# Kernel tuning notes

Measured on AMD Instinct MI355X. Metric: run time of the kernel, lower is better.

Reference implementation:

```python
import jax, jax.numpy as jnp
import numpy as np

N, D, R, B, K = 16384, 300, 10, 1024, 64


def setup_inputs() -> dict:
    key = jax.random.key(0)
    ks = jax.random.split(key, 6)
    return {
        "node_feat_src": jax.random.normal(ks[0], (N, D), jnp.float32),
        "node_feat_tgt": jax.random.normal(ks[1], (N, D), jnp.float32),
        "srcs_index": jax.random.randint(ks[2], (B, K), 0, N),
        "tgts_index": jax.random.randint(ks[3], (B, K), 0, N),
        "src_vs": jax.random.normal(ks[4], (R, D), jnp.float32),
        "tgt_vs": jax.random.normal(ks[5], (R, D), jnp.float32),
    }


def _tower(h, vs):
    # Householder chain: h @ (I - v v^T / (v^T v)) == h - ((h v) / (v^T v)) v^T
    def step(h, v):
        coef = (h @ v) / (v @ v)  # [N]
        return h - coef[:, None] * v[None, :], None
    h, _ = jax.lax.scan(step, h, vs)
    return h


def _l2norm(x):
    # matches F.normalize(p=2, eps=1e-12) over the last dim
    n = jnp.linalg.norm(x, axis=-1, keepdims=True)
    return x / jnp.maximum(n, 1e-12)


def reference(node_feat_src, node_feat_tgt, srcs_index, tgts_index, src_vs, tgt_vs):
    src_h = _tower(node_feat_src, src_vs)  # [N, D]
    tgt_h = _tower(node_feat_tgt, tgt_vs)  # [N, D]

    pos_src = _l2norm(src_h[srcs_index[:, 0]])  # [B, D]
    pos_tgt = _l2norm(tgt_h[tgts_index[:, 0]])  # [B, D]
    src_list = _l2norm(src_h[srcs_index])       # [B, K, D]
    tgt_list = _l2norm(tgt_h[tgts_index])       # [B, K, D]

    sim_src2tgt = jnp.einsum('bd,bkd->bk', pos_src, tgt_list)  # [B, K]
    sim_tgt2src = jnp.einsum('bd,bkd->bk', pos_tgt, src_list)  # [B, K]

    # CSLS hubness penalties: mean of top-10 cross-domain cosine sims
    sim_matrix = _l2norm(src_h) @ _l2norm(tgt_h).T  # [N, N]
    rt = jnp.mean(jax.lax.top_k(sim_matrix, 10)[0], axis=1)    # [N]
    rs = jnp.mean(jax.lax.top_k(sim_matrix.T, 10)[0], axis=1)  # [N]

    srcs_rt = rt[srcs_index]  # [B, K]
    tgts_rs = rs[tgts_index]  # [B, K]

    logits_src2tgt = sim_src2tgt * 2 - srcs_rt[:, 0:1] - tgts_rs
    logits_tgt2src = sim_tgt2src * 2 - tgts_rs[:, 0:1] - srcs_rt
    return logits_src2tgt, logits_tgt2src
```

## Files before the change

### kernel.cpp

```cpp
#include <hip/hip_runtime.h>
#include <hip/hip_bf16.h>

#define NN 16384
#define DD 300
#define DP 320
#define RR 10
#define BB 1024
#define KK 64
#define CAP 128
#define CAPL 512

typedef __attribute__((ext_vector_type(8))) short s8v;
typedef __attribute__((ext_vector_type(4))) float f4v;
typedef _Float16 h2 __attribute__((ext_vector_type(2)));

__device__ __forceinline__ unsigned mono2(unsigned d) {
    unsigned s = ((d >> 15) & 0x10001u) * 0xFFFFu;
    return d ^ (s | 0x80008000u);
}
__device__ __forceinline__ float key2f16(unsigned k) {
    unsigned short b = (k & 0x8000u) ? (unsigned short)(k ^ 0x8000u)
                                     : (unsigned short)(~k & 0xFFFFu);
    _Float16 hv = __builtin_bit_cast(_Float16, b);
    return (float)hv;
}

__device__ __forceinline__ h2 h2max(h2 a, h2 b) {
    return __builtin_elementwise_max(a, b);
}
__device__ __forceinline__ h2 hmax2s(h2 a, int xb) {
    int x = __shfl_xor(__builtin_bit_cast(int, a), xb);
    return h2max(a, __builtin_bit_cast(h2, x));
}
__device__ __forceinline__ h2 packh2(float a, float b) {
    h2 r; r[0] = (_Float16)a; r[1] = (_Float16)b; return r;
}

__device__ __forceinline__ void ins10(unsigned (&lst)[10], unsigned v) {
    #pragma unroll
    for (int q = 0; q < 10; ++q) {
        unsigned a  = lst[q];
        unsigned mx = a > v ? a : v;
        v           = a > v ? v : a;
        lst[q] = mx;
    }
}
__device__ __forceinline__ void ins10f(float (&lst)[10], float v) {
    #pragma unroll
    for (int q = 0; q < 10; ++q) {
        float a  = lst[q];
        float mx = fmaxf(a, v);
        v        = fminf(a, v);
        lst[q] = mx;
    }
}

__device__ __forceinline__ void xcd_map(int bid, int& by, int& bx) {
    const int xcd = bid & 7;
    const int s   = bid >> 3;
    bx = (xcd << 2) | (s & 3);
    by = s >> 2;
}

__device__ __forceinline__ void gload_lds16(const void* g, void* l) {
#if __has_builtin(__builtin_amdgcn_global_load_lds)
    __builtin_amdgcn_global_load_lds(
        (const __attribute__((address_space(1))) void*)g,
        (__attribute__((address_space(3))) void*)l, 16, 0, 0);
#else
    const int lane = threadIdx.x & 63;
    int4 v = *reinterpret_cast<const int4*>(g);
    *reinterpret_cast<int4*>((char*)l + lane * 16) = v;
#endif
}

__device__ __forceinline__ void stage_tile(
        const __hip_bfloat16* __restrict__ Ab, const __hip_bfloat16* __restrict__ Bb,
        int kb, char* base, int w, int lane) {
    const int r8 = lane >> 3;
    const int u  = (lane & 7) ^ r8;
    const int row = w * 8 + r8;
    const size_t go = (size_t)row * DP + kb * 64 + u * 8;
    gload_lds16(Ab + go, base + w * 1024);
    gload_lds16(Bb + go, base + 16384 + w * 1024);
}

__global__ __launch_bounds__(256) void tower_kernel(
        const float* __restrict__ feat, const float* __restrict__ vs,
        __hip_bfloat16* __restrict__ out) {
    __shared__ float vsh[RR * DD];
    const int tid = threadIdx.x;
    for (int i = tid; i < RR * DD; i += 256) vsh[i] = vs[i];
    __syncthreads();

    const int lane = tid & 63;
    const int wave = tid >> 6;
    const int row  = blockIdx.x * 4 + wave;

    float h[5];
    #pragma unroll
    for (int j = 0; j < 5; ++j) {
        int d = lane + 64 * j;
        h[j] = (d < DD) ? feat[(size_t)row * DD + d] : 0.f;
    }
    #pragma unroll
    for (int r = 0; r < RR; ++r) {
        float vl[5];
        float hv = 0.f, vv = 0.f;
        #pragma unroll
        for (int j = 0; j < 5; ++j) {
            int d = lane + 64 * j;
            float v = (d < DD) ? vsh[r * DD + d] : 0.f;
            vl[j] = v;
            hv += h[j] * v;
            vv += v * v;
        }
        #pragma unroll
        for (int o = 32; o; o >>= 1) {
            hv += __shfl_xor(hv, o);
            vv += __shfl_xor(vv, o);
        }
        float coef = hv / vv;
        #pragma unroll
        for (int j = 0; j < 5; ++j) h[j] -= coef * vl[j];
    }
    float nn = 0.f;
    #pragma unroll
    for (int j = 0; j < 5; ++j) nn += h[j] * h[j];
    #pragma unroll
    for (int o = 32; o; o >>= 1) nn += __shfl_xor(nn, o);
    float scale = 1.f / fmaxf(sqrtf(nn), 1e-12f);
    #pragma unroll
    for (int j = 0; j < 5; ++j) {
        int d = lane + 64 * j;
        float val = (d < DD) ? h[j] * scale : 0.f;
        out[(size_t)row * DP + d] = __float2bfloat16(val);
    }
}

#define KLOOP(COMPUTE_BODY)                                                    \
    stage_tile(Ab, Bb, 0, u_lds, w, lane);                                     \
    _Pragma("unroll")                                                          \
    for (int kb = 0; kb < 5; ++kb) {                                           \
        char* curb = u_lds + (kb & 1) * 32768;                                 \
        if (kb < 4)                                                            \
            stage_tile(Ab, Bb, kb + 1, u_lds + ((kb + 1) & 1) * 32768, w, lane); \
        if (kb < 4) { asm volatile("s_waitcnt vmcnt(2)" ::: "memory"); }       \
        else        { asm volatile("s_waitcnt vmcnt(0)" ::: "memory"); }       \
        __builtin_amdgcn_s_barrier();                                          \
        asm volatile("" ::: "memory");                                         \
        {                                                                      \
            const __hip_bfloat16* Asub = (const __hip_bfloat16*)curb;          \
            const __hip_bfloat16* Bsub = (const __hip_bfloat16*)(curb + 16384);\
            COMPUTE_BODY                                                       \
        }                                                                      \
        asm volatile("" ::: "memory");                                         \
        __builtin_amdgcn_s_barrier();                                          \
    }

#define COMPUTE_TILE                                                           \
    _Pragma("unroll")                                                          \
    for (int ks = 0; ks < 2; ++ks) {                                           \
        s8v af[2], bfv[2];                                                     \
        const int ulog = ks * 4 + (lane >> 4);                                 \
        const int up   = ulog ^ (lane & 7);                                    \
        _Pragma("unroll")                                                      \
        for (int m = 0; m < 2; ++m) {                                          \
            const int row = wr * 32 + m * 16 + (lane & 15);                    \
            af[m] = *reinterpret_cast<const s8v*>(Asub + row * 64 + up * 8);   \
        }                                                                      \
        _Pragma("unroll")                                                      \
        for (int n = 0; n < 2; ++n) {                                          \
            const int row = wc * 32 + n * 16 + (lane & 15);                    \
            bfv[n] = *reinterpret_cast<const s8v*>(Bsub + row * 64 + up * 8);  \
        }                                                                      \
        _Pragma("unroll")                                                      \
        for (int m = 0; m < 2; ++m)                                            \
            _Pragma("unroll")                                                  \
            for (int n = 0; n < 2; ++n)                                        \
                acc[m][n] = __builtin_amdgcn_mfma_f32_16x16x32_bf16(           \
                    af[m], bfv[n], acc[m][n], 0, 0, 0);                        \
    }

__global__ __launch_bounds__(1024) void passA_kernel(
        const __hip_bfloat16* __restrict__ A, const __hip_bfloat16* __restrict__ Bm,
        unsigned short* __restrict__ rowsmax_g,
        unsigned short* __restrict__ colsmax_g) {
    __shared__ __align__(16) char u_lds[65536];
    __shared__ unsigned short rowsm[16][512];
    __shared__ unsigned short colsm[512][16];

    const int tid = threadIdx.x;
    const int lane = tid & 63;
    const int w = tid >> 6;
    const int wr = w >> 2, wc = w & 3;
    int by, bx; xcd_map(blockIdx.x, by, bx);
    const int i0 = by * 512, j0 = bx * 512;

    for (int ti = 0; ti < 4; ++ti) {
        for (int tj = 0; tj < 4; ++tj) {
            f4v acc[2][2];
            #pragma unroll
            for (int m = 0; m < 2; ++m)
                #pragma unroll
                for (int n = 0; n < 2; ++n)
                    acc[m][n] = (f4v){0.f, 0.f, 0.f, 0.f};

            const __hip_bfloat16* Ab = A  + (size_t)(i0 + ti * 128) * DP;
            const __hip_bfloat16* Bb = Bm + (size_t)(j0 + tj * 128) * DP;

            KLOOP(COMPUTE_TILE)

            #pragma unroll
            for (int m = 0; m < 2; ++m) {
                h2 a01 = h2max(packh2(acc[m][0][0], acc[m][0][1]),
                               packh2(acc[m][1][0], acc[m][1][1]));
                h2 a23 = h2max(packh2(acc[m][0][2], acc[m][0][3]),
                               packh2(acc[m][1][2], acc[m][1][3]));
                a01 = hmax2s(a01, 1); a23 = hmax2s(a23, 1);
                a01 = hmax2s(a01, 2); a23 = hmax2s(a23, 2);
                a01 = hmax2s(a01, 4); a23 = hmax2s(a23, 4);
                a01 = hmax2s(a01, 8); a23 = hmax2s(a23, 8);
                if ((lane & 15) == m * 8) {
                    const int rl = ti * 128 + wr * 32 + m * 16 + ((lane >> 4) << 2);
                    uint2 u = make_uint2(mono2(__builtin_bit_cast(unsigned, a01)),
                                         mono2(__builtin_bit_cast(unsigned, a23)));
                    *reinterpret_cast<uint2*>(&rowsm[tj * 4 + wc][rl]) = u;
                }
            }
            {
                float rm0 = -1e30f, rm1 = -1e30f;
                #pragma unroll
                for (int m = 0; m < 2; ++m) {
                    rm0 = fmaxf(rm0, fmaxf(fmaxf(acc[m][0][0], acc[m][0][1]),
                                           fmaxf(acc[m][0][2], acc[m][0][3])));
                    rm1 = fmaxf(rm1, fmaxf(fmaxf(acc[m][1][0], acc[m][1][1]),
                                           fmaxf(acc[m][1][2], acc[m][1][3])));
                }
                h2 c = packh2(rm0, rm1);
                c = hmax2s(c, 16);
                c = hmax2s(c, 32);
                if ((lane >> 4) == 0) {
                    const int s = ti * 4 + wr;
                    const int cb = tj * 128 + wc * 32 + (lane & 15);
                    unsigned k = mono2(__builtin_bit_cast(unsigned, c));
                    colsm[cb][s]      = (unsigned short)(k & 0xFFFFu);
                    colsm[cb + 16][s] = (unsigned short)(k >> 16);
                }
            }
        }
    }
    __syncthreads();
    if (tid < 512) {
        const int r = tid;
        unsigned short t16[16];
        #pragma unroll
        for (int s = 0; s < 16; ++s) t16[s] = rowsm[s][r];
        uint4 o0, o1;
        o0.x = t16[0] | ((unsigned)t16[1] << 16);  o0.y = t16[2] | ((unsigned)t16[3] << 16);
        o0.z = t16[4] | ((unsigned)t16[5] << 16);  o0.w = t16[6] | ((unsigned)t16[7] << 16);
        o1.x = t16[8] | ((unsigned)t16[9] << 16);  o1.y = t16[10] | ((unsigned)t16[11] << 16);
        o1.z = t16[12] | ((unsigned)t16[13] << 16); o1.w = t16[14] | ((unsigned)t16[15] << 16);
        uint4* rdst = reinterpret_cast<uint4*>(rowsmax_g + (size_t)(i0 + r) * 512 + bx * 16);
        rdst[0] = o0; rdst[1] = o1;
    } else {
        const int r = tid - 512;
        uint4 q0 = *reinterpret_cast<uint4*>(&colsm[r][0]);
        uint4 q1 = *reinterpret_cast<uint4*>(&colsm[r][8]);
        uint4* cdst = reinterpret_cast<uint4*>(colsmax_g + (size_t)(j0 + r) * 512 + by * 16);
        cdst[0] = q0; cdst[1] = q1;
    }
}

__global__ __launch_bounds__(256) void thresh_kernel(
        const unsigned short* __restrict__ rowsmax_g,
        const unsigned short* __restrict__ colsmax_g,
        float* __restrict__ Tlb_row, float* __restrict__ Tlb_col,
        unsigned* __restrict__ rowcnt, unsigned* __restrict__ colcnt) {
    const int t = blockIdx.x * 256 + threadIdx.x;
    const bool isRow = t < NN;
    const int idx = isRow ? t : t - NN;
    const unsigned short* src = (isRow ? rowsmax_g : colsmax_g) + (size_t)idx * 512;

    unsigned lst[10];
    #pragma unroll
    for (int q = 0; q < 10; ++q) lst[q] = 0u;

    const uint4* p = reinterpret_cast<const uint4*>(src);
    for (int c = 0; c < 64; ++c) {
        uint4 q = p[c];
        unsigned v0 = q.x & 0xFFFFu, v1 = q.x >> 16;
        unsigned v2 = q.y & 0xFFFFu, v3 = q.y >> 16;
        unsigned v4 = q.z & 0xFFFFu, v5 = q.z >> 16;
        unsigned v6 = q.w & 0xFFFFu, v7 = q.w >> 16;
        unsigned g01 = v0 > v1 ? v0 : v1, g23 = v2 > v3 ? v2 : v3;
        unsigned g45 = v4 > v5 ? v4 : v5, g67 = v6 > v7 ? v6 : v7;
        unsigned ga = g01 > g23 ? g01 : g23, gb = g45 > g67 ? g45 : g67;
        unsigned g = ga > gb ? ga : gb;
        if (g > lst[9]) {
            if (v0 > lst[9]) ins10(lst, v0);
            if (v1 > lst[9]) ins10(lst, v1);
            if (v2 > lst[9]) ins10(lst, v2);
            if (v3 > lst[9]) ins10(lst, v3);
            if (v4 > lst[9]) ins10(lst, v4);
            if (v5 > lst[9]) ins10(lst, v5);
            if (v6 > lst[9]) ins10(lst, v6);
            if (v7 > lst[9]) ins10(lst, v7);
        }
    }
    float f = key2f16(lst[9]);
    float lb = f - fabsf(f) * 0.002f - 1e-6f;
    if (isRow) { Tlb_row[idx] = lb; rowcnt[idx] = 0u; }
    else       { Tlb_col[idx] = lb; colcnt[idx] = 0u; }
}

__global__ __launch_bounds__(1024) void passB_kernel(
        const __hip_bfloat16* __restrict__ A, const __hip_bfloat16* __restrict__ Bm,
        const float* __restrict__ Tlb_row, const float* __restrict__ Tlb_col,
        unsigned* __restrict__ rowcnt, unsigned* __restrict__ colcnt,
        float* __restrict__ rowbuf, float* __restrict__ colbuf) {
    __shared__ __align__(16) char u_lds[65536];
    __shared__ float Trow_s[512];
    __shared__ float Tcol_s[512];
    __shared__ unsigned scnt[2];
    __shared__ uint2 sbuf[2][CAPL];

    const int tid = threadIdx.x;
    const int lane = tid & 63;
    const int w = tid >> 6;
    const int wr = w >> 2, wc = w & 3;
    int by, bx; xcd_map(blockIdx.x, by, bx);
    const int i0 = by * 512, j0 = bx * 512;

    if (tid < 512) Trow_s[tid] = Tlb_row[i0 + tid];
    else           Tcol_s[tid - 512] = Tlb_col[j0 + tid - 512];
    if (tid < 2) scnt[tid] = 0u;
    __syncthreads();

    for (int ti = 0; ti < 4; ++ti) {
        float trmin = 1e30f;
        #pragma unroll
        for (int m = 0; m < 2; ++m)
            #pragma unroll
            for (int r = 0; r < 4; ++r)
                trmin = fminf(trmin, Trow_s[ti * 128 + wr * 32 + m * 16 + ((lane >> 4) << 2) + r]);

        for (int tj = 0; tj < 4; ++tj) {
            f4v acc[2][2];
            #pragma unroll
            for (int m = 0; m < 2; ++m)
                #pragma unroll
                for (int n = 0; n < 2; ++n)
                    acc[m][n] = (f4v){0.f, 0.f, 0.f, 0.f};

            const __hip_bfloat16* Ab = A  + (size_t)(i0 + ti * 128) * DP;
            const __hip_bfloat16* Bb = Bm + (size_t)(j0 + tj * 128) * DP;

            KLOOP(COMPUTE_TILE)

            const int c0i = tj * 128 + wc * 32 + (lane & 15);
            const int c1i = c0i + 16;
            const float tc0 = Tcol_s[c0i], tc1 = Tcol_s[c1i];
            float vm = -1e30f;
            #pragma unroll
            for (int m = 0; m < 2; ++m) {
                float a = fmaxf(fmaxf(acc[m][0][0], acc[m][0][1]),
                                fmaxf(acc[m][0][2], acc[m][0][3]));
                float b = fmaxf(fmaxf(acc[m][1][0], acc[m][1][1]),
                                fmaxf(acc[m][1][2], acc[m][1][3]));
                vm = fmaxf(vm, fmaxf(a, b));
            }
            if (vm >= fminf(trmin, fminf(tc0, tc1))) {
                #pragma unroll
                for (int m = 0; m < 2; ++m) {
                    #pragma unroll
                    for (int r = 0; r < 4; ++r) {
                        const int rl = ti * 128 + wr * 32 + m * 16 + ((lane >> 4) << 2) + r;
                        const float T = Trow_s[rl];
                        const float v0 = acc[m][0][r], v1 = acc[m][1][r];
                        if (v0 >= T) {
                            unsigned p = atomicAdd(&scnt[0], 1u);
                            if (p < CAPL) sbuf[0][p] = make_uint2((unsigned)(i0 + rl), __float_as_uint(v0));
                            else { unsigned q = atomicAdd(&rowcnt[i0 + rl], 1u);
                                   if (q < CAP) rowbuf[(size_t)(i0 + rl) * CAP + q] = v0; }
                        }
                        if (v1 >= T) {
                            unsigned p = atomicAdd(&scnt[0], 1u);
                            if (p < CAPL) sbuf[0][p] = make_uint2((unsigned)(i0 + rl), __float_as_uint(v1));
                            else { unsigned q = atomicAdd(&rowcnt[i0 + rl], 1u);
                                   if (q < CAP) rowbuf[(size_t)(i0 + rl) * CAP + q] = v1; }
                        }
                        if (v0 >= tc0) {
                            unsigned p = atomicAdd(&scnt[1], 1u);
                            if (p < CAPL) sbuf[1][p] = make_uint2((unsigned)(j0 + c0i), __float_as_uint(v0));
                            else { unsigned q = atomicAdd(&colcnt[j0 + c0i], 1u);
                                   if (q < CAP) colbuf[(size_t)(j0 + c0i) * CAP + q] = v0; }
                        }
                        if (v1 >= tc1) {
                            unsigned p = atomicAdd(&scnt[1], 1u);
                            if (p < CAPL) sbuf[1][p] = make_uint2((unsigned)(j0 + c1i), __float_as_uint(v1));
                            else { unsigned q = atomicAdd(&colcnt[j0 + c1i], 1u);
                                   if (q < CAP) colbuf[(size_t)(j0 + c1i) * CAP + q] = v1; }
                        }
                    }
                }
            }
        }
    }

    __syncthreads();
    {
        const unsigned nr = scnt[0] < CAPL ? scnt[0] : CAPL;
        const unsigned nc = scnt[1] < CAPL ? scnt[1] : CAPL;
        for (unsigned i = tid; i < nr; i += 1024) {
            uint2 e = sbuf[0][i];
            unsigned p = atomicAdd(&rowcnt[e.x], 1u);
            if (p < CAP) rowbuf[(size_t)e.x * CAP + p] = __uint_as_float(e.y);
        }
        for (unsigned i = tid; i < nc; i += 1024) {
            uint2 e = sbuf[1][i];
            unsigned p = atomicAdd(&colcnt[e.x], 1u);
            if (p < CAP) colbuf[(size_t)e.x * CAP + p] = __uint_as_float(e.y);
        }
    }
}

__global__ __launch_bounds__(256) void final_kernel(
        const unsigned* __restrict__ rowcnt, const unsigned* __restrict__ colcnt,
        const float* __restrict__ rowbuf, const float* __restrict__ colbuf,
        float* __restrict__ rt, float* __restrict__ rs) {
    const int t = blockIdx.x * 256 + threadIdx.x;
    const bool isRow = t < NN;
    const int idx = isRow ? t : t - NN;
    const unsigned cn = (isRow ? rowcnt : colcnt)[idx];
    const int n = (int)(cn < CAP ? cn : CAP);
    const float* buf = (isRow ? rowbuf : colbuf) + (size_t)idx * CAP;

    float lst[10];
    #pragma unroll
    for (int q = 0; q < 10; ++q) lst[q] = -1e30f;
    for (int i = 0; i < n; ++i) {
        float v = buf[i];
        if (v > lst[9]) ins10f(lst, v);
    }
    float s = 0.f;
    #pragma unroll
    for (int q = 0; q < 10; ++q) s += lst[q];
    s *= 0.1f;
    (isRow ? rt : rs)[idx] = s;
}

__global__ __launch_bounds__(256) void logits_kernel(
        const __hip_bfloat16* __restrict__ srcH, const __hip_bfloat16* __restrict__ tgtH,
        const int* __restrict__ sidx, const int* __restrict__ tidx,
        const float* __restrict__ rt, const float* __restrict__ rs,
        float* __restrict__ out) {
    const int b    = blockIdx.x;
    const int lane = threadIdx.x & 63;
    const int w    = threadIdx.x >> 6;

    const int s0 = sidx[b * KK];
    const int t0 = tidx[b * KK];
    float ps[5], pt[5];
    #pragma unroll
    for (int j = 0; j < 5; ++j) {
        int d = lane + 64 * j;
        ps[j] = __bfloat162float(srcH[(size_t)s0 * DP + d]);
        pt[j] = __bfloat162float(tgtH[(size_t)t0 * DP + d]);
    }
    const float rt_s0 = rt[s0];
    const float rs_t0 = rs[t0];

    for (int kk = w; kk < KK; kk += 4) {
        const int it = tidx[b * KK + kk];
        const int is = sidx[b * KK + kk];
        float a = 0.f, c = 0.f;
        #pragma unroll
        for (int j = 0; j < 5; ++j) {
            int d = lane + 64 * j;
            a += ps[j] * __bfloat162float(tgtH[(size_t)it * DP + d]);
            c += pt[j] * __bfloat162float(srcH[(size_t)is * DP + d]);
        }
        #pragma unroll
        for (int o = 32; o; o >>= 1) {
            a += __shfl_xor(a, o);
            c += __shfl_xor(c, o);
        }
        if (lane == 0) {
            out[b * KK + kk]           = 2.f * a - rt_s0 - rs[it];
            out[BB * KK + b * KK + kk] = 2.f * c - rs_t0 - rt[is];
        }
    }
}

extern "C" void kernel_launch(void* const* d_in, const int* in_sizes, int n_in,
                              void* d_out, int out_size, void* d_ws, size_t ws_size,
                              hipStream_t stream) {
    const float* nf_src = (const float*)d_in[0];
    const float* nf_tgt = (const float*)d_in[1];
    const int*   sidx   = (const int*)d_in[2];
    const int*   tidx   = (const int*)d_in[3];
    const float* svs    = (const float*)d_in[4];
    const float* tvs    = (const float*)d_in[5];

    char* ws = (char*)d_ws;
    const size_t SZ_H  = (size_t)NN * DP * 2;
    const size_t SZ_SM = (size_t)NN * 512 * 2;
    __hip_bfloat16* srcH = (__hip_bfloat16*)ws;
    __hip_bfloat16* tgtH = (__hip_bfloat16*)(ws + SZ_H);
    unsigned short* rowsmax = (unsigned short*)(ws + 2 * SZ_H);
    unsigned short* colsmax = (unsigned short*)(ws + 2 * SZ_H + SZ_SM);
    float* rowbuf = (float*)(ws + 2 * SZ_H);
    float* colbuf = (float*)(ws + 2 * SZ_H + (size_t)NN * CAP * 4);
    char* tail = ws + 2 * SZ_H + 2 * SZ_SM;
    float* Tlb_row = (float*)(tail);
    float* Tlb_col = (float*)(tail + 65536);
    unsigned* rowcnt = (unsigned*)(tail + 2 * 65536);
    unsigned* colcnt = (unsigned*)(tail + 3 * 65536);
    float* rt = (float*)(tail + 4 * 65536);
    float* rs = (float*)(tail + 5 * 65536);

    tower_kernel<<<NN / 4, 256, 0, stream>>>(nf_src, svs, srcH);
    tower_kernel<<<NN / 4, 256, 0, stream>>>(nf_tgt, tvs, tgtH);
    passA_kernel<<<1024, 1024, 0, stream>>>(srcH, tgtH, rowsmax, colsmax);
    thresh_kernel<<<(2 * NN) / 256, 256, 0, stream>>>(rowsmax, colsmax, Tlb_row, Tlb_col,
                                                      rowcnt, colcnt);
    passB_kernel<<<1024, 1024, 0, stream>>>(srcH, tgtH, Tlb_row, Tlb_col,
                                            rowcnt, colcnt, rowbuf, colbuf);
    final_kernel<<<(2 * NN) / 256, 256, 0, stream>>>(rowcnt, colcnt, rowbuf, colbuf, rt, rs);
    logits_kernel<<<BB, 256, 0, stream>>>(srcH, tgtH, sidx, tidx, rt, rs, (float*)d_out);
}
```

Before: 632.8 us.

## Compute two column tiles per K-loop to reuse A tile and halve barriers

Both GEMM passes now process a pair of 128-column B tiles per K-loop iteration, staging A once alongside two B tiles in a larger double-buffered LDS region. This reuses A fragments across twice the MFMAs and halves the number of barrier-synchronised K-loops and A reloads. The cost is more accumulator registers and LDS per block (96KB staging plus existing buffers), which may pressure occupancy or exceed LDS limits alongside the other shared arrays.

```diff
diff --git a/kernel.cpp b/kernel.cpp
--- a/kernel.cpp
+++ b/kernel.cpp
@@ -9,6 +9,7 @@
 #define KK 64
 #define CAP 128
 #define CAPL 512
+#define BUFSZ 49152
 
 typedef __attribute__((ext_vector_type(8))) short s8v;
 typedef __attribute__((ext_vector_type(4))) float f4v;
@@ -74,15 +75,18 @@
 #endif
 }
 
-__device__ __forceinline__ void stage_tile(
-        const __hip_bfloat16* __restrict__ Ab, const __hip_bfloat16* __restrict__ Bb,
+__device__ __forceinline__ void stage_tile2(
+        const __hip_bfloat16* __restrict__ Ab,
+        const __hip_bfloat16* __restrict__ Bb0,
+        const __hip_bfloat16* __restrict__ Bb1,
         int kb, char* base, int w, int lane) {
     const int r8 = lane >> 3;
     const int u  = (lane & 7) ^ r8;
     const int row = w * 8 + r8;
     const size_t go = (size_t)row * DP + kb * 64 + u * 8;
-    gload_lds16(Ab + go, base + w * 1024);
-    gload_lds16(Bb + go, base + 16384 + w * 1024);
+    gload_lds16(Ab  + go, base + w * 1024);
+    gload_lds16(Bb0 + go, base + 16384 + w * 1024);
+    gload_lds16(Bb1 + go, base + 32768 + w * 1024);
 }
 
 __global__ __launch_bounds__(256) void tower_kernel(
@@ -138,55 +142,96 @@
     }
 }
 
-#define KLOOP(COMPUTE_BODY)                                                    \
-    stage_tile(Ab, Bb, 0, u_lds, w, lane);                                     \
+#define KLOOP2                                                                 \
+    stage_tile2(Ab, Bb0, Bb1, 0, u_lds, w, lane);                              \
     _Pragma("unroll")                                                          \
     for (int kb = 0; kb < 5; ++kb) {                                           \
-        char* curb = u_lds + (kb & 1) * 32768;                                 \
+        char* curb = u_lds + (kb & 1) * BUFSZ;                                 \
         if (kb < 4)                                                            \
-            stage_tile(Ab, Bb, kb + 1, u_lds + ((kb + 1) & 1) * 32768, w, lane); \
-        if (kb < 4) { asm volatile("s_waitcnt vmcnt(2)" ::: "memory"); }       \
+            stage_tile2(Ab, Bb0, Bb1, kb + 1, u_lds + ((kb + 1) & 1) * BUFSZ, w, lane); \
+        if (kb < 4) { asm volatile("s_waitcnt vmcnt(3)" ::: "memory"); }       \
         else        { asm volatile("s_waitcnt vmcnt(0)" ::: "memory"); }       \
         __builtin_amdgcn_s_barrier();                                          \
         asm volatile("" ::: "memory");                                         \
         {                                                                      \
-            const __hip_bfloat16* Asub = (const __hip_bfloat16*)curb;          \
-            const __hip_bfloat16* Bsub = (const __hip_bfloat16*)(curb + 16384);\
-            COMPUTE_BODY                                                       \
+            const __hip_bfloat16* Asub  = (const __hip_bfloat16*)curb;         \
+            const __hip_bfloat16* B0sub = (const __hip_bfloat16*)(curb + 16384); \
+            const __hip_bfloat16* B1sub = (const __hip_bfloat16*)(curb + 32768); \
+            _Pragma("unroll")                                                  \
+            for (int ks = 0; ks < 2; ++ks) {                                   \
+                s8v af[2], bf0[2], bf1[2];                                     \
+                const int ulog = ks * 4 + (lane >> 4);                         \
+                const int up   = ulog ^ (lane & 7);                            \
+                _Pragma("unroll")                                              \
+                for (int m = 0; m < 2; ++m) {                                  \
+                    const int row = wr * 32 + m * 16 + (lane & 15);            \
+                    af[m] = *reinterpret_cast<const s8v*>(Asub + row * 64 + up * 8); \
+                }                                                              \
+                _Pragma("unroll")                                              \
+                for (int n = 0; n < 2; ++n) {                                  \
+                    const int row = wc * 32 + n * 16 + (lane & 15);            \
+                    bf0[n] = *reinterpret_cast<const s8v*>(B0sub + row * 64 + up * 8); \
+                    bf1[n] = *reinterpret_cast<const s8v*>(B1sub + row * 64 + up * 8); \
+                }                                                              \
+                _Pragma("unroll")                                              \
+                for (int m = 0; m < 2; ++m)                                    \
+                    _Pragma("unroll")                                          \
+                    for (int n = 0; n < 2; ++n) {                              \
+                        acc0[m][n] = __builtin_amdgcn_mfma_f32_16x16x32_bf16(  \
+                            af[m], bf0[n], acc0[m][n], 0, 0, 0);               \
+                        acc1[m][n] = __builtin_amdgcn_mfma_f32_16x16x32_bf16(  \
+                            af[m], bf1[n], acc1[m][n], 0, 0, 0);               \
+                    }                                                          \
+            }                                                                  \
         }                                                                      \
         asm volatile("" ::: "memory");                                         \
         __builtin_amdgcn_s_barrier();                                          \
     }
 
-#define COMPUTE_TILE                                                           \
+#define ROWCOL_EPI(ACC, TJ)                                                    \
     _Pragma("unroll")                                                          \
-    for (int ks = 0; ks < 2; ++ks) {                                           \
-        s8v af[2], bfv[2];                                                     \
-        const int ulog = ks * 4 + (lane >> 4);                                 \
-        const int up   = ulog ^ (lane & 7);                                    \
+    for (int m = 0; m < 2; ++m) {                                              \
+        h2 a01 = h2max(packh2(ACC[m][0][0], ACC[m][0][1]),                     \
+                       packh2(ACC[m][1][0], ACC[m][1][1]));                    \
+        h2 a23 = h2max(packh2(ACC[m][0][2], ACC[m][0][3]),                     \
+                       packh2(ACC[m][1][2], ACC[m][1][3]));                    \
+        a01 = hmax2s(a01, 1); a23 = hmax2s(a23, 1);                            \
+        a01 = hmax2s(a01, 2); a23 = hmax2s(a23, 2);                            \
+        a01 = hmax2s(a01, 4); a23 = hmax2s(a23, 4);                            \
+        a01 = hmax2s(a01, 8); a23 = hmax2s(a23, 8);                            \
+        if ((lane & 15) == m * 8) {                                            \
+            const int rl = ti * 128 + wr * 32 + m * 16 + ((lane >> 4) << 2);   \
+            uint2 u = make_uint2(mono2(__builtin_bit_cast(unsigned, a01)),     \
+                                 mono2(__builtin_bit_cast(unsigned, a23)));    \
+            *reinterpret_cast<uint2*>(&rowsm[(TJ) * 4 + wc][rl]) = u;          \
+        }                                                                      \
+    }                                                                          \
+    {                                                                          \
+        float rm0 = -1e30f, rm1 = -1e30f;                                      \
         _Pragma("unroll")                                                      \
         for (int m = 0; m < 2; ++m) {                                          \
-            const int row = wr * 32 + m * 16 + (lane & 15);                    \
-            af[m] = *reinterpret_cast<const s8v*>(Asub + row * 64 + up * 8);   \
+            rm0 = fmaxf(rm0, fmaxf(fmaxf(ACC[m][0][0], ACC[m][0][1]),          \
+                                   fmaxf(ACC[m][0][2], ACC[m][0][3])));        \
+            rm1 = fmaxf(rm1, fmaxf(fmaxf(ACC[m][1][0], ACC[m][1][1]),          \
+                                   fmaxf(ACC[m][1][2], ACC[m][1][3])));        \
         }                                                                      \
-        _Pragma("unroll")                                                      \
-        for (int n = 0; n < 2; ++n) {                                          \
-            const int row = wc * 32 + n * 16 + (lane & 15);                    \
-            bfv[n] = *reinterpret_cast<const s8v*>(Bsub + row * 64 + up * 8);  \
+        h2 c = packh2(rm0, rm1);                                               \
+        c = hmax2s(c, 16);                                                     \
+        c = hmax2s(c, 32);                                                     \
+        if ((lane >> 4) == 0) {                                                \
+            const int s = ti * 4 + wr;                                         \
+            const int cb = (TJ) * 128 + wc * 32 + (lane & 15);                 \
+            unsigned k = mono2(__builtin_bit_cast(unsigned, c));               \
+            colsm[cb][s]      = (unsigned short)(k & 0xFFFFu);                 \
+            colsm[cb + 16][s] = (unsigned short)(k >> 16);                     \
         }                                                                      \
-        _Pragma("unroll")                                                      \
-        for (int m = 0; m < 2; ++m)                                            \
-            _Pragma("unroll")                                                  \
-            for (int n = 0; n < 2; ++n)                                        \
-                acc[m][n] = __builtin_amdgcn_mfma_f32_16x16x32_bf16(           \
-                    af[m], bfv[n], acc[m][n], 0, 0, 0);                        \
     }
 
 __global__ __launch_bounds__(1024) void passA_kernel(
         const __hip_bfloat16* __restrict__ A, const __hip_bfloat16* __restrict__ Bm,
         unsigned short* __restrict__ rowsmax_g,
         unsigned short* __restrict__ colsmax_g) {
-    __shared__ __align__(16) char u_lds[65536];
+    __shared__ __align__(16) char u_lds[2 * BUFSZ];
     __shared__ unsigned short rowsm[16][512];
     __shared__ unsigned short colsm[512][16];
 
@@ -198,56 +243,25 @@
     const int i0 = by * 512, j0 = bx * 512;
 
     for (int ti = 0; ti < 4; ++ti) {
-        for (int tj = 0; tj < 4; ++tj) {
-            f4v acc[2][2];
+        for (int tjp = 0; tjp < 2; ++tjp) {
+            const int tj0 = tjp * 2, tj1 = tjp * 2 + 1;
+            f4v acc0[2][2], acc1[2][2];
             #pragma unroll
             for (int m = 0; m < 2; ++m)
                 #pragma unroll
-                for (int n = 0; n < 2; ++n)
-                    acc[m][n] = (f4v){0.f, 0.f, 0.f, 0.f};
-
-            const __hip_bfloat16* Ab = A  + (size_t)(i0 + ti * 128) * DP;
-            const __hip_bfloat16* Bb = Bm + (size_t)(j0 + tj * 128) * DP;
-
-            KLOOP(COMPUTE_TILE)
-
-            #pragma unroll
-            for (int m = 0; m < 2; ++m) {
-                h2 a01 = h2max(packh2(acc[m][0][0], acc[m][0][1]),
-                               packh2(acc[m][1][0], acc[m][1][1]));
-                h2 a23 = h2max(packh2(acc[m][0][2], acc[m][0][3]),
-                               packh2(acc[m][1][2], acc[m][1][3]));
-                a01 = hmax2s(a01, 1); a23 = hmax2s(a23, 1);
-                a01 = hmax2s(a01, 2); a23 = hmax2s(a23, 2);
-                a01 = hmax2s(a01, 4); a23 = hmax2s(a23, 4);
-                a01 = hmax2s(a01, 8); a23 = hmax2s(a23, 8);
-                if ((lane & 15) == m * 8) {
-                    const int rl = ti * 128 + wr * 32 + m * 16 + ((lane >> 4) << 2);
-                    uint2 u = make_uint2(mono2(__builtin_bit_cast(unsigned, a01)),
-                                         mono2(__builtin_bit_cast(unsigned, a23)));
-                    *reinterpret_cast<uint2*>(&rowsm[tj * 4 + wc][rl]) = u;
+                for (int n = 0; n < 2; ++n) {
+                    acc0[m][n] = (f4v){0.f, 0.f, 0.f, 0.f};
+                    acc1[m][n] = (f4v){0.f, 0.f, 0.f, 0.f};
                 }
-            }
-            {
-                float rm0 = -1e30f, rm1 = -1e30f;
-                #pragma unroll
-                for (int m = 0; m < 2; ++m) {
-                    rm0 = fmaxf(rm0, fmaxf(fmaxf(acc[m][0][0], acc[m][0][1]),
-                                           fmaxf(acc[m][0][2], acc[m][0][3])));
-                    rm1 = fmaxf(rm1, fmaxf(fmaxf(acc[m][1][0], acc[m][1][1]),
-                                           fmaxf(acc[m][1][2], acc[m][1][3])));
-                }
-                h2 c = packh2(rm0, rm1);
-                c = hmax2s(c, 16);
-                c = hmax2s(c, 32);
-                if ((lane >> 4) == 0) {
-                    const int s = ti * 4 + wr;
-                    const int cb = tj * 128 + wc * 32 + (lane & 15);
-                    unsigned k = mono2(__builtin_bit_cast(unsigned, c));
-                    colsm[cb][s]      = (unsigned short)(k & 0xFFFFu);
-                    colsm[cb + 16][s] = (unsigned short)(k >> 16);
-                }
-            }
+
+            const __hip_bfloat16* Ab  = A  + (size_t)(i0 + ti * 128) * DP;
+            const __hip_bfloat16* Bb0 = Bm + (size_t)(j0 + tj0 * 128) * DP;
+            const __hip_bfloat16* Bb1 = Bm + (size_t)(j0 + tj1 * 128) * DP;
+
+            KLOOP2
+
+            ROWCOL_EPI(acc0, tj0)
+            ROWCOL_EPI(acc1, tj1)
         }
     }
     __syncthreads();
@@ -314,12 +328,63 @@
     else       { Tlb_col[idx] = lb; colcnt[idx] = 0u; }
 }
 
+#define FILTER_EPI(ACC, TJ)                                                    \
+    {                                                                          \
+        const int c0i = (TJ) * 128 + wc * 32 + (lane & 15);                    \
+        const int c1i = c0i + 16;                                              \
+        const float tc0 = Tcol_s[c0i], tc1 = Tcol_s[c1i];                      \
+        float vm = -1e30f;                                                     \
+        _Pragma("unroll")                                                      \
+        for (int m = 0; m < 2; ++m) {                                          \
+            float a = fmaxf(fmaxf(ACC[m][0][0], ACC[m][0][1]),                 \
+                            fmaxf(ACC[m][0][2], ACC[m][0][3]));                \
+            float b = fmaxf(fmaxf(ACC[m][1][0], ACC[m][1][1]),                 \
+                            fmaxf(ACC[m][1][2], ACC[m][1][3]));                \
+            vm = fmaxf(vm, fmaxf(a, b));                                       \
+        }                                                                      \
+        if (vm >= fminf(trmin, fminf(tc0, tc1))) {                             \
+            _Pragma("unroll")                                                  \
+            for (int m = 0; m < 2; ++m) {                                      \
+                _Pragma("unroll")                                              \
+                for (int r = 0; r < 4; ++r) {                                  \
+                    const int rl = ti * 128 + wr * 32 + m * 16 + ((lane >> 4) << 2) + r; \
+                    const float T = Trow_s[rl];                                \
+                    const float v0 = ACC[m][0][r], v1 = ACC[m][1][r];          \
+                    if (v0 >= T) {                                             \
+                        unsigned p = atomicAdd(&scnt[0], 1u);                  \
+                        if (p < CAPL) sbuf[0][p] = make_uint2((unsigned)(i0 + rl), __float_as_uint(v0)); \
+                        else { unsigned q = atomicAdd(&rowcnt[i0 + rl], 1u);   \
+                               if (q < CAP) rowbuf[(size_t)(i0 + rl) * CAP + q] = v0; } \
+                    }                                                          \
+                    if (v1 >= T) {                                             \
+                        unsigned p = atomicAdd(&scnt[0], 1u);                  \
+                        if (p < CAPL) sbuf[0][p] = make_uint2((unsigned)(i0 + rl), __float_as_uint(v1)); \
+                        else { unsigned q = atomicAdd(&rowcnt[i0 + rl], 1u);   \
+                               if (q < CAP) rowbuf[(size_t)(i0 + rl) * CAP + q] = v1; } \
+                    }                                                          \
+                    if (v0 >= tc0) {                                           \
+                        unsigned p = atomicAdd(&scnt[1], 1u);                  \
+                        if (p < CAPL) sbuf[1][p] = make_uint2((unsigned)(j0 + c0i), __float_as_uint(v0)); \
+                        else { unsigned q = atomicAdd(&colcnt[j0 + c0i], 1u);  \
+                               if (q < CAP) colbuf[(size_t)(j0 + c0i) * CAP + q] = v0; } \
+                    }                                                          \
+                    if (v1 >= tc1) {                                           \
+                        unsigned p = atomicAdd(&scnt[1], 1u);                  \
+                        if (p < CAPL) sbuf[1][p] = make_uint2((unsigned)(j0 + c1i), __float_as_uint(v1)); \
+                        else { unsigned q = atomicAdd(&colcnt[j0 + c1i], 1u);  \
+                               if (q < CAP) colbuf[(size_t)(j0 + c1i) * CAP + q] = v1; } \
+                    }                                                          \
+                }                                                              \
+            }                                                                  \
+        }                                                                      \
+    }
+
 __global__ __launch_bounds__(1024) void passB_kernel(
         const __hip_bfloat16* __restrict__ A, const __hip_bfloat16* __restrict__ Bm,
         const float* __restrict__ Tlb_row, const float* __restrict__ Tlb_col,
         unsigned* __restrict__ rowcnt, unsigned* __restrict__ colcnt,
         float* __restrict__ rowbuf, float* __restrict__ colbuf) {
-    __shared__ __align__(16) char u_lds[65536];
+    __shared__ __align__(16) char u_lds[2 * BUFSZ];
     __shared__ float Trow_s[512];
     __shared__ float Tcol_s[512];
     __shared__ unsigned scnt[2];
@@ -345,66 +410,25 @@
             for (int r = 0; r < 4; ++r)
                 trmin = fminf(trmin, Trow_s[ti * 128 + wr * 32 + m * 16 + ((lane >> 4) << 2) + r]);
 
-        for (int tj = 0; tj < 4; ++tj) {
-            f4v acc[2][2];
+        for (int tjp = 0; tjp < 2; ++tjp) {
+            const int tj0 = tjp * 2, tj1 = tjp * 2 + 1;
+            f4v acc0[2][2], acc1[2][2];
             #pragma unroll
             for (int m = 0; m < 2; ++m)
                 #pragma unroll
-                for (int n = 0; n < 2; ++n)
-                    acc[m][n] = (f4v){0.f, 0.f, 0.f, 0.f};
-
-            const __hip_bfloat16* Ab = A  + (size_t)(i0 + ti * 128) * DP;
-            const __hip_bfloat16* Bb = Bm + (size_t)(j0 + tj * 128) * DP;
-
-            KLOOP(COMPUTE_TILE)
-
-            const int c0i = tj * 128 + wc * 32 + (lane & 15);
-            const int c1i = c0i + 16;
-            const float tc0 = Tcol_s[c0i], tc1 = Tcol_s[c1i];
-            float vm = -1e30f;
-            #pragma unroll
-            for (int m = 0; m < 2; ++m) {
-                float a = fmaxf(fmaxf(acc[m][0][0], acc[m][0][1]),
-                                fmaxf(acc[m][0][2], acc[m][0][3]));
-                float b = fmaxf(fmaxf(acc[m][1][0], acc[m][1][1]),
-                                fmaxf(acc[m][1][2], acc[m][1][3]));
-                vm = fmaxf(vm, fmaxf(a, b));
-            }
-            if (vm >= fminf(trmin, fminf(tc0, tc1))) {
-                #pragma unroll
-                for (int m = 0; m < 2; ++m) {
-                    #pragma unroll
-                    for (int r = 0; r < 4; ++r) {
-                        const int rl = ti * 128 + wr * 32 + m * 16 + ((lane >> 4) << 2) + r;
-                        const float T = Trow_s[rl];
-                        const float v0 = acc[m][0][r], v1 = acc[m][1][r];
-                        if (v0 >= T) {
-                            unsigned p = atomicAdd(&scnt[0], 1u);
-                            if (p < CAPL) sbuf[0][p] = make_uint2((unsigned)(i0 + rl), __float_as_uint(v0));
-                            else { unsigned q = atomicAdd(&rowcnt[i0 + rl], 1u);
-                                   if (q < CAP) rowbuf[(size_t)(i0 + rl) * CAP + q] = v0; }
-                        }
-                        if (v1 >= T) {
-                            unsigned p = atomicAdd(&scnt[0], 1u);
-                            if (p < CAPL) sbuf[0][p] = make_uint2((unsigned)(i0 + rl), __float_as_uint(v1));
-                            else { unsigned q = atomicAdd(&rowcnt[i0 + rl], 1u);
-                                   if (q < CAP) rowbuf[(size_t)(i0 + rl) * CAP + q] = v1; }
-                        }
-                        if (v0 >= tc0) {
-                            unsigned p = atomicAdd(&scnt[1], 1u);
-                            if (p < CAPL) sbuf[1][p] = make_uint2((unsigned)(j0 + c0i), __float_as_uint(v0));
-                            else { unsigned q = atomicAdd(&colcnt[j0 + c0i], 1u);
-                                   if (q < CAP) colbuf[(size_t)(j0 + c0i) * CAP + q] = v0; }
-                        }
-                        if (v1 >= tc1) {
-                            unsigned p = atomicAdd(&scnt[1], 1u);
-                            if (p < CAPL) sbuf[1][p] = make_uint2((unsigned)(j0 + c1i), __float_as_uint(v1));
-                            else { unsigned q = atomicAdd(&colcnt[j0 + c1i], 1u);
-                                   if (q < CAP) colbuf[(size_t)(j0 + c1i) * CAP + q] = v1; }
-                        }
-                    }
+                for (int n = 0; n < 2; ++n) {
+                    acc0[m][n] = (f4v){0.f, 0.f, 0.f, 0.f};
+                    acc1[m][n] = (f4v){0.f, 0.f, 0.f, 0.f};
                 }
-            }
+
+            const __hip_bfloat16* Ab  = A  + (size_t)(i0 + ti * 128) * DP;
+            const __hip_bfloat16* Bb0 = Bm + (size_t)(j0 + tj0 * 128) * DP;
+            const __hip_bfloat16* Bb1 = Bm + (size_t)(j0 + tj1 * 128) * DP;
+
+            KLOOP2
+
+            FILTER_EPI(acc0, tj0)
+            FILTER_EPI(acc1, tj1)
         }
     }
 
```

Result: faster. 616.7 us (-2.5%).
